# Kernel optimization log

Measured on AMD Instinct MI355X. Metric: run time of the kernel, lower is better.

The kernel has to match this reference:

```python
import jax, jax.numpy as jnp
import numpy as np

S, B, H = 2048, 16, 1024


def setup_inputs() -> dict:
    key = jax.random.key(0)
    k1, k2, k3, k4 = jax.random.split(key, 4)
    encoder_output = jax.random.normal(k1, (S, B, H), dtype=jnp.float32)
    last_decoder_state = jax.random.normal(k2, (2, 1, B, H), dtype=jnp.float32)
    W = jax.random.normal(k3, (H, H), dtype=jnp.float32) * (1.0 / np.sqrt(H))
    b = jax.random.normal(k4, (H,), dtype=jnp.float32) * 0.01
    return {"encoder_output": encoder_output, "last_decoder_state": last_decoder_state, "W": W, "b": b}


def reference(encoder_output, last_decoder_state, W, b):
    # state = last_decoder_state[0] -> [1, B, H]; Linear applied to it, then squeeze(0)
    state = last_decoder_state[0, 0]              # [B, H]
    energy = state @ W.T + b                      # [B, H]  (nn.Linear)
    # per-timestep bmm == batched dot of each encoder step with energy
    scores = jnp.einsum("sbh,bh->sb", encoder_output, energy)  # [S, B]
    sm = jax.nn.softmax(scores, axis=0)           # softmax over seq dim
    return sm[None, None]                          # [1, 1, S, B]
```

## Files before the change

kernel.cpp:

```cpp
#include <hip/hip_runtime.h>

#define SEQ 2048
#define BATCH 16
#define HID 1024

__global__ __launch_bounds__(256) void energy_kernel(
    const float* __restrict__ state,
    const float* __restrict__ W,
    const float* __restrict__ bias,
    float* __restrict__ energy)
{
    const int wave = threadIdx.x >> 6;
    const int lane = threadIdx.x & 63;
    const int o = blockIdx.x * 4 + wave;
    const int b = o >> 10;
    const int h = o & (HID - 1);

    const float4* __restrict__ wrow = reinterpret_cast<const float4*>(W + (size_t)h * HID);
    const float4* __restrict__ srow = reinterpret_cast<const float4*>(state + (size_t)b * HID);

    float sum = 0.0f;
#pragma unroll
    for (int it = 0; it < HID / 4 / 64; ++it) {
        const int idx = it * 64 + lane;
        const float4 w4 = wrow[idx];
        const float4 s4 = srow[idx];
        sum = fmaf(w4.x, s4.x, sum);
        sum = fmaf(w4.y, s4.y, sum);
        sum = fmaf(w4.z, s4.z, sum);
        sum = fmaf(w4.w, s4.w, sum);
    }
#pragma unroll
    for (int off = 32; off > 0; off >>= 1) sum += __shfl_down(sum, off);
    if (lane == 0) energy[o] = sum + bias[h];
}

__global__ __launch_bounds__(256) void scores_kernel(
    const float* __restrict__ enc,
    const float* __restrict__ energy,
    float* __restrict__ scores)
{
    const int wave = threadIdx.x >> 6;
    const int lane = threadIdx.x & 63;
    const int o = blockIdx.x * 4 + wave;
    const int b = o & (BATCH - 1);

    const float4* __restrict__ erow = reinterpret_cast<const float4*>(enc + (size_t)o * HID);
    const float4* __restrict__ grow = reinterpret_cast<const float4*>(energy + (size_t)b * HID);

    float sum = 0.0f;
#pragma unroll
    for (int it = 0; it < HID / 4 / 64; ++it) {
        const int idx = it * 64 + lane;
        const float4 e4 = erow[idx];
        const float4 g4 = grow[idx];
        sum = fmaf(e4.x, g4.x, sum);
        sum = fmaf(e4.y, g4.y, sum);
        sum = fmaf(e4.z, g4.z, sum);
        sum = fmaf(e4.w, g4.w, sum);
    }
#pragma unroll
    for (int off = 32; off > 0; off >>= 1) sum += __shfl_down(sum, off);
    if (lane == 0) scores[o] = sum;
}

__global__ __launch_bounds__(256) void softmax_kernel(
    const float* __restrict__ scores,
    float* __restrict__ out)
{
    const int b = blockIdx.x;
    const int t = threadIdx.x;

    float vals[SEQ / 256];
    float m = -INFINITY;
#pragma unroll
    for (int i = 0; i < SEQ / 256; ++i) {
        vals[i] = scores[(size_t)(t + i * 256) * BATCH + b];
        m = fmaxf(m, vals[i]);
    }

    __shared__ float redm[4];
#pragma unroll
    for (int off = 32; off > 0; off >>= 1) m = fmaxf(m, __shfl_xor(m, off));
    if ((t & 63) == 0) redm[t >> 6] = m;
    __syncthreads();
    m = fmaxf(fmaxf(redm[0], redm[1]), fmaxf(redm[2], redm[3]));

    float lsum = 0.0f;
#pragma unroll
    for (int i = 0; i < SEQ / 256; ++i) {
        vals[i] = expf(vals[i] - m);
        lsum += vals[i];
    }

    __shared__ float reds[4];
#pragma unroll
    for (int off = 32; off > 0; off >>= 1) lsum += __shfl_xor(lsum, off);
    if ((t & 63) == 0) reds[t >> 6] = lsum;
    __syncthreads();
    const float inv = 1.0f / (reds[0] + reds[1] + reds[2] + reds[3]);

#pragma unroll
    for (int i = 0; i < SEQ / 256; ++i)
        out[(size_t)(t + i * 256) * BATCH + b] = vals[i] * inv;
}

extern "C" void kernel_launch(void* const* d_in, const int* in_sizes, int n_in,
                              void* d_out, int out_size, void* d_ws, size_t ws_size,
                              hipStream_t stream) {
    const float* enc   = (const float*)d_in[0];
    const float* lds   = (const float*)d_in[1];
    const float* W     = (const float*)d_in[2];
    const float* bias  = (const float*)d_in[3];
    float* out = (float*)d_out;

    float* energy = (float*)d_ws;
    float* scores = energy + BATCH * HID;

    energy_kernel<<<BATCH * HID / 4, 256, 0, stream>>>(lds, W, bias, energy);
    scores_kernel<<<SEQ * BATCH / 4, 256, 0, stream>>>(enc, energy, scores);
    softmax_kernel<<<BATCH, 256, 0, stream>>>(scores, out);
}
```

Baseline: 202.7 us.

## Process four seq rows per wave and transpose scores for coalesced softmax

Each wave in the scores kernel now computes four sequence positions for one batch, holding the energy vector in registers and reusing it across the four rows. This cuts the grid to a quarter of its size. Scores are written transposed as [B, S] with float4 stores, so the softmax kernel can read each batch row with contiguous float4 loads instead of strided ones. The output writes stay strided, and the extra registers may lower occupancy.

```diff
diff --git a/kernel.cpp b/kernel.cpp
--- a/kernel.cpp
+++ b/kernel.cpp
@@ -38,46 +38,57 @@
 __global__ __launch_bounds__(256) void scores_kernel(
     const float* __restrict__ enc,
     const float* __restrict__ energy,
-    float* __restrict__ scores)
+    float* __restrict__ scoresT)
 {
     const int wave = threadIdx.x >> 6;
     const int lane = threadIdx.x & 63;
-    const int o = blockIdx.x * 4 + wave;
-    const int b = o & (BATCH - 1);
+    const int w = blockIdx.x * 4 + wave;
+    const int b = w & (BATCH - 1);
+    const int s0 = (w >> 4) * 4;
 
-    const float4* __restrict__ erow = reinterpret_cast<const float4*>(enc + (size_t)o * HID);
     const float4* __restrict__ grow = reinterpret_cast<const float4*>(energy + (size_t)b * HID);
+    float4 g[4];
+#pragma unroll
+    for (int it = 0; it < 4; ++it) g[it] = grow[it * 64 + lane];
 
-    float sum = 0.0f;
+    float sum[4] = {0.f, 0.f, 0.f, 0.f};
 #pragma unroll
-    for (int it = 0; it < HID / 4 / 64; ++it) {
-        const int idx = it * 64 + lane;
-        const float4 e4 = erow[idx];
-        const float4 g4 = grow[idx];
-        sum = fmaf(e4.x, g4.x, sum);
-        sum = fmaf(e4.y, g4.y, sum);
-        sum = fmaf(e4.z, g4.z, sum);
-        sum = fmaf(e4.w, g4.w, sum);
+    for (int r = 0; r < 4; ++r) {
+        const float4* __restrict__ erow =
+            reinterpret_cast<const float4*>(enc + ((size_t)(s0 + r) * BATCH + b) * HID);
+#pragma unroll
+        for (int it = 0; it < 4; ++it) {
+            const float4 e = erow[it * 64 + lane];
+            sum[r] = fmaf(e.x, g[it].x, sum[r]);
+            sum[r] = fmaf(e.y, g[it].y, sum[r]);
+            sum[r] = fmaf(e.z, g[it].z, sum[r]);
+            sum[r] = fmaf(e.w, g[it].w, sum[r]);
+        }
     }
 #pragma unroll
-    for (int off = 32; off > 0; off >>= 1) sum += __shfl_down(sum, off);
-    if (lane == 0) scores[o] = sum;
+    for (int r = 0; r < 4; ++r) {
+#pragma unroll
+        for (int off = 32; off > 0; off >>= 1) sum[r] += __shfl_down(sum[r], off);
+    }
+    if (lane == 0) {
+        float4 v = make_float4(sum[0], sum[1], sum[2], sum[3]);
+        *reinterpret_cast<float4*>(scoresT + (size_t)b * SEQ + s0) = v;
+    }
 }
 
 __global__ __launch_bounds__(256) void softmax_kernel(
-    const float* __restrict__ scores,
+    const float* __restrict__ scoresT,
     float* __restrict__ out)
 {
     const int b = blockIdx.x;
     const int t = threadIdx.x;
+    const float4* __restrict__ row = reinterpret_cast<const float4*>(scoresT + (size_t)b * SEQ);
 
-    float vals[SEQ / 256];
-    float m = -INFINITY;
-#pragma unroll
-    for (int i = 0; i < SEQ / 256; ++i) {
-        vals[i] = scores[(size_t)(t + i * 256) * BATCH + b];
-        m = fmaxf(m, vals[i]);
-    }
+    float4 v0 = row[t];
+    float4 v1 = row[t + 256];
+
+    float m = fmaxf(fmaxf(fmaxf(v0.x, v0.y), fmaxf(v0.z, v0.w)),
+                    fmaxf(fmaxf(v1.x, v1.y), fmaxf(v1.z, v1.w)));
 
     __shared__ float redm[4];
 #pragma unroll
@@ -86,12 +97,12 @@
     __syncthreads();
     m = fmaxf(fmaxf(redm[0], redm[1]), fmaxf(redm[2], redm[3]));
 
-    float lsum = 0.0f;
-#pragma unroll
-    for (int i = 0; i < SEQ / 256; ++i) {
-        vals[i] = expf(vals[i] - m);
-        lsum += vals[i];
-    }
+    v0.x = expf(v0.x - m); v0.y = expf(v0.y - m);
+    v0.z = expf(v0.z - m); v0.w = expf(v0.w - m);
+    v1.x = expf(v1.x - m); v1.y = expf(v1.y - m);
+    v1.z = expf(v1.z - m); v1.w = expf(v1.w - m);
+
+    float lsum = (v0.x + v0.y + v0.z + v0.w) + (v1.x + v1.y + v1.z + v1.w);
 
     __shared__ float reds[4];
 #pragma unroll
@@ -100,9 +111,16 @@
     __syncthreads();
     const float inv = 1.0f / (reds[0] + reds[1] + reds[2] + reds[3]);
 
-#pragma unroll
-    for (int i = 0; i < SEQ / 256; ++i)
-        out[(size_t)(t + i * 256) * BATCH + b] = vals[i] * inv;
+    const int s0 = t * 4;
+    out[(size_t)(s0 + 0) * BATCH + b] = v0.x * inv;
+    out[(size_t)(s0 + 1) * BATCH + b] = v0.y * inv;
+    out[(size_t)(s0 + 2) * BATCH + b] = v0.z * inv;
+    out[(size_t)(s0 + 3) * BATCH + b] = v0.w * inv;
+    const int s1 = (t + 256) * 4;
+    out[(size_t)(s1 + 0) * BATCH + b] = v1.x * inv;
+    out[(size_t)(s1 + 1) * BATCH + b] = v1.y * inv;
+    out[(size_t)(s1 + 2) * BATCH + b] = v1.z * inv;
+    out[(size_t)(s1 + 3) * BATCH + b] = v1.w * inv;
 }
 
 extern "C" void kernel_launch(void* const* d_in, const int* in_sizes, int n_in,
@@ -114,10 +132,10 @@
     const float* bias  = (const float*)d_in[3];
     float* out = (float*)d_out;
 
-    float* energy = (float*)d_ws;
-    float* scores = energy + BATCH * HID;
+    float* energy  = (float*)d_ws;
+    float* scoresT = energy + BATCH * HID;
 
     energy_kernel<<<BATCH * HID / 4, 256, 0, stream>>>(lds, W, bias, energy);
-    scores_kernel<<<SEQ * BATCH / 4, 256, 0, stream>>>(enc, energy, scores);
-    softmax_kernel<<<BATCH, 256, 0, stream>>>(scores, out);
+    scores_kernel<<<SEQ * BATCH / 4 / 4, 256, 0, stream>>>(enc, energy, scoresT);
+    softmax_kernel<<<BATCH, 256, 0, stream>>>(scoresT, out);
 }
```

Result: no change. 199.9 us (-1.4%).
